# Kernel optimization log

Measured on AMD Instinct MI355X. Metric: run time of the kernel, lower is better.

## Reference

```python
import jax, jax.numpy as jnp
import numpy as np

N = 100000      # nodes
E = 1600000     # directed edges
LAT = 128
MAT = 8
OUT = 3


def setup_inputs() -> dict:
    key = jax.random.key(0)
    ks = jax.random.split(key, 5)
    z = jax.random.normal(ks[0], (N, LAT), dtype=jnp.float32)
    material_params = jax.random.normal(ks[1], (N, MAT), dtype=jnp.float32)
    edge_index = jax.random.randint(ks[2], (2, E), 0, N, dtype=jnp.int64)
    W1 = jax.random.normal(ks[3], (LAT + MAT, LAT), dtype=jnp.float32) * 0.05
    b1 = jnp.zeros((LAT,), dtype=jnp.float32)
    W2 = jax.random.normal(ks[4], (LAT, OUT), dtype=jnp.float32) * 0.05
    b2 = jnp.zeros((OUT,), dtype=jnp.float32)
    return {"z": z, "edge_index": edge_index, "material_params": material_params,
            "W1": W1, "b1": b1, "W2": W2, "b2": b2}


def _gcn_norm(edge_index, num_nodes):
    # PyG GCNConv default: add self-loops, symmetric normalization
    src, dst = edge_index[0], edge_index[1]
    loop = jnp.arange(num_nodes, dtype=src.dtype)
    row = jnp.concatenate([src, loop])  # message source
    col = jnp.concatenate([dst, loop])  # message target
    deg = jax.ops.segment_sum(jnp.ones_like(col, dtype=jnp.float32), col,
                              num_segments=num_nodes)
    dinv = jnp.where(deg > 0, jax.lax.rsqrt(deg), 0.0)
    norm = dinv[row] * dinv[col]        # [E + N]
    return row, col, norm


def _gcn_conv(x, W, b, row, col, norm, num_nodes):
    h = x @ W                                   # linear first (PyG order)
    msg = h[row] * norm[:, None]                # gather + scale
    agg = jax.ops.segment_sum(msg, col, num_segments=num_nodes)
    return agg + b


def reference(z, edge_index, material_params, W1, b1, W2, b2):
    row, col, norm = _gcn_norm(edge_index, N)
    x = jnp.concatenate([z, material_params], axis=1)     # [N, LAT+MAT]
    x = jax.nn.relu(_gcn_conv(x, W1, b1, row, col, norm, N))
    x = _gcn_conv(x, W2, b2, row, col, norm, N)           # [N, OUT]
    return x
```

## Files before the change

### kernel.cpp

```cpp
#include <hip/hip_runtime.h>

#define N_NODES 100000
#define N_EDGES 1600000
#define LAT 128
#define MAT 8
#define OUTC 3

#define NBKT 391
#define CAP  4608
#define CHUNK 4096
#define NPART 8

typedef __attribute__((ext_vector_type(8))) short bf16x8;
typedef __attribute__((ext_vector_type(4))) float f32x4;

__device__ __forceinline__ unsigned short bf16r(float f) {
    unsigned int u = __float_as_uint(f);
    u = (u + 0x7fffu + ((u >> 16) & 1u)) >> 16;
    return (unsigned short)u;
}
__device__ __forceinline__ float bf16f(unsigned short h) {
    return __uint_as_float((unsigned int)h << 16);
}

__global__ __launch_bounds__(256) void k_binA(const int* __restrict__ src,
                                              const int* __restrict__ dst,
                                              int* __restrict__ gcount,
                                              unsigned int* __restrict__ binned) {
    __shared__ int hist[NBKT];
    __shared__ int adj[NBKT];
    __shared__ int cur[NBKT];
    __shared__ int wsum[4];
    __shared__ unsigned int lbuf[CHUNK];
    __shared__ unsigned short lbkt[CHUNK];

    int t = threadIdx.x;
    int base = blockIdx.x * CHUNK;
    int nEdge = min(CHUNK, N_EDGES - base);

    for (int i = t; i < NBKT; i += 256) hist[i] = 0;
    __syncthreads();

    unsigned int pk[16];
    unsigned short bk[16];
#pragma unroll
    for (int j = 0; j < 16; ++j) {
        int li = j * 256 + t;
        if (li < nEdge) {
            int e = base + li;
            int d = dst[e];
            int s = src[e];
            pk[j] = ((unsigned int)s << 8) | (unsigned int)(d & 255);
            bk[j] = (unsigned short)(d >> 8);
            atomicAdd(&hist[bk[j]], 1);
        } else {
            bk[j] = 0xffffu;
        }
    }
    __syncthreads();

    int lane = t & 63, w = t >> 6;
    int i0 = 2 * t, i1 = 2 * t + 1;
    int h0 = (i0 < NBKT) ? hist[i0] : 0;
    int h1 = (i1 < NBKT) ? hist[i1] : 0;
    int ps = h0 + h1;
    int x = ps;
#pragma unroll
    for (int off = 1; off < 64; off <<= 1) {
        int y = __shfl_up(x, off, 64);
        if (lane >= off) x += y;
    }
    if (lane == 63) wsum[w] = x;
    __syncthreads();
    int woff = 0;
#pragma unroll
    for (int i = 0; i < 4; ++i)
        if (i < w) woff += wsum[i];
    int excl = woff + x - ps;
    if (i0 < NBKT) {
        int g0 = i0 * CAP + atomicAdd(&gcount[i0], h0);
        adj[i0] = g0 - excl;
        cur[i0] = excl;
    }
    if (i1 < NBKT) {
        int g1r = i1 * CAP + atomicAdd(&gcount[i1], h1);
        adj[i1] = g1r - (excl + h0);
        cur[i1] = excl + h0;
    }
    __syncthreads();

#pragma unroll
    for (int j = 0; j < 16; ++j) {
        if (bk[j] != 0xffffu) {
            int pos = atomicAdd(&cur[bk[j]], 1);
            lbuf[pos] = pk[j];
            lbkt[pos] = bk[j];
        }
    }
    __syncthreads();

    for (int i = t; i < nEdge; i += 256) {
        int b = lbkt[i];
        binned[adj[b] + i] = lbuf[i];
    }
}

__global__ __launch_bounds__(256) void k_bscan(const int* __restrict__ gcount,
                                               int* __restrict__ bucketBase,
                                               int* __restrict__ rowptr) {
    __shared__ int wsum[4];
    int t = threadIdx.x;
    int lane = t & 63, w = t >> 6;
    int i0 = 2 * t, i1 = 2 * t + 1;
    int h0 = (i0 < NBKT) ? gcount[i0] : 0;
    int h1 = (i1 < NBKT) ? gcount[i1] : 0;
    int ps = h0 + h1;
    int x = ps;
#pragma unroll
    for (int off = 1; off < 64; off <<= 1) {
        int y = __shfl_up(x, off, 64);
        if (lane >= off) x += y;
    }
    if (lane == 63) wsum[w] = x;
    __syncthreads();
    int woff = 0;
#pragma unroll
    for (int i = 0; i < 4; ++i)
        if (i < w) woff += wsum[i];
    int excl = woff + x - ps;
    bucketBase[i0] = excl;
    bucketBase[i1] = excl + h0;
    if (t == 0) rowptr[N_NODES] = N_EDGES;
}

__global__ __launch_bounds__(256) void k_binB(const unsigned int* __restrict__ binned,
                                              const int* __restrict__ gcount,
                                              const int* __restrict__ bucketBase,
                                              int* __restrict__ colsrc,
                                              int* __restrict__ rowptr,
                                              float* __restrict__ dinv) {
    __shared__ unsigned int lbuf[CAP];
    __shared__ int lsrc[CAP];
    __shared__ int hist[256];
    __shared__ int cur[256];
    __shared__ int wsum[4];

    int b = blockIdx.x, t = threadIdx.x;
    int cnt = min(gcount[b], CAP);
    int gb = bucketBase[b];
    const unsigned int* bp = binned + (size_t)b * CAP;

    for (int i = t; i < cnt; i += 256) lbuf[i] = bp[i];
    hist[t] = 0;
    __syncthreads();
    for (int i = t; i < cnt; i += 256) atomicAdd(&hist[lbuf[i] & 255], 1);
    __syncthreads();

    int lane = t & 63, w = t >> 6;
    int h = hist[t];
    int x = h;
#pragma unroll
    for (int off = 1; off < 64; off <<= 1) {
        int y = __shfl_up(x, off, 64);
        if (lane >= off) x += y;
    }
    if (lane == 63) wsum[w] = x;
    __syncthreads();
    int woff = 0;
#pragma unroll
    for (int i = 0; i < 4; ++i)
        if (i < w) woff += wsum[i];
    int excl = woff + x - h;
    cur[t] = excl;

    int node = b * 256 + t;
    if (node < N_NODES) {
        rowptr[node] = gb + excl;
        dinv[node] = rsqrtf((float)h + 1.0f);
    }
    __syncthreads();

    for (int i = t; i < cnt; i += 256) {
        unsigned int p = lbuf[i];
        int pos = atomicAdd(&cur[p & 255], 1);
        lsrc[pos] = (int)(p >> 8);
    }
    __syncthreads();

    for (int i = t; i < cnt; i += 256) colsrc[gb + i] = lsrc[i];
}

__global__ void k_wsplit(const float* __restrict__ W1,
                         unsigned short* __restrict__ w1h,
                         unsigned short* __restrict__ w1l) {
    int i = blockIdx.x * 256 + threadIdx.x;
    if (i >= 160 * 128) return;
    int k = i >> 7;
    float w = (k < LAT + MAT) ? W1[i] : 0.f;
    unsigned short h = bf16r(w);
    w1h[i] = h;
    w1l[i] = bf16r(w - bf16f(h));
}

__global__ __launch_bounds__(256) void k_gemm1m(const float* __restrict__ z,
                                                const float* __restrict__ mat,
                                                const unsigned short* __restrict__ w1h,
                                                const unsigned short* __restrict__ w1l,
                                                const float* __restrict__ dinv,
                                                unsigned short* __restrict__ g1p) {
    int wv = threadIdx.x >> 6;
    int l = threadIdx.x & 63;
    int lm = l & 15, q = l >> 4;

    bf16x8 bh[2][5], bl[2][5];
#pragma unroll
    for (int ct = 0; ct < 2; ++ct) {
        int col = (wv * 2 + ct) * 16 + lm;
#pragma unroll
        for (int ks = 0; ks < 5; ++ks) {
#pragma unroll
            for (int j = 0; j < 8; ++j) {
                int k = ks * 32 + q * 8 + j;
                bh[ct][ks][j] = (short)w1h[k * 128 + col];
                bl[ct][ks][j] = (short)w1l[k * 128 + col];
            }
        }
    }

    for (int tile = blockIdx.x; tile < N_NODES / 16; tile += gridDim.x) {
        int n0 = tile * 16;
        int row = n0 + lm;
        f32x4 acc0 = {0.f, 0.f, 0.f, 0.f};
        f32x4 acc1 = {0.f, 0.f, 0.f, 0.f};
#pragma unroll
        for (int ks = 0; ks < 5; ++ks) {
            float a[8];
            if (ks < 4) {
                float4 a0 = *(const float4*)&z[(size_t)row * LAT + ks * 32 + q * 8];
                float4 a1 = *(const float4*)&z[(size_t)row * LAT + ks * 32 + q * 8 + 4];
                a[0] = a0.x; a[1] = a0.y; a[2] = a0.z; a[3] = a0.w;
                a[4] = a1.x; a[5] = a1.y; a[6] = a1.z; a[7] = a1.w;
            } else if (q == 0) {
                float4 m0 = *(const float4*)&mat[(size_t)row * MAT];
                float4 m1 = *(const float4*)&mat[(size_t)row * MAT + 4];
                a[0] = m0.x; a[1] = m0.y; a[2] = m0.z; a[3] = m0.w;
                a[4] = m1.x; a[5] = m1.y; a[6] = m1.z; a[7] = m1.w;
            } else {
#pragma unroll
                for (int j = 0; j < 8; ++j) a[j] = 0.f;
            }
            bf16x8 ah, al;
#pragma unroll
            for (int j = 0; j < 8; ++j) {
                unsigned short h = bf16r(a[j]);
                ah[j] = (short)h;
                al[j] = (short)bf16r(a[j] - bf16f(h));
            }
            acc0 = __builtin_amdgcn_mfma_f32_16x16x32_bf16(ah, bh[0][ks], acc0, 0, 0, 0);
            acc1 = __builtin_amdgcn_mfma_f32_16x16x32_bf16(ah, bh[1][ks], acc1, 0, 0, 0);
            acc0 = __builtin_amdgcn_mfma_f32_16x16x32_bf16(al, bh[0][ks], acc0, 0, 0, 0);
            acc1 = __builtin_amdgcn_mfma_f32_16x16x32_bf16(al, bh[1][ks], acc1, 0, 0, 0);
            acc0 = __builtin_amdgcn_mfma_f32_16x16x32_bf16(ah, bl[0][ks], acc0, 0, 0, 0);
            acc1 = __builtin_amdgcn_mfma_f32_16x16x32_bf16(ah, bl[1][ks], acc1, 0, 0, 0);
        }
#pragma unroll
        for (int r = 0; r < 4; ++r) {
            int m = q * 4 + r;
            float d = dinv[n0 + m];
            g1p[(size_t)(wv * 2 + 0) * (N_NODES * 16) + (size_t)(n0 + m) * 16 + lm] = bf16r(acc0[r] * d);
            g1p[(size_t)(wv * 2 + 1) * (N_NODES * 16) + (size_t)(n0 + m) * 16 + lm] = bf16r(acc1[r] * d);
        }
    }
}

__global__ __launch_bounds__(256) void k_gather1p(const unsigned int* __restrict__ g1p,
                                                  const int* __restrict__ colsrc,
                                                  const int* __restrict__ rowptr,
                                                  const float* __restrict__ dinv,
                                                  const float* __restrict__ b1,
                                                  const float* __restrict__ W2,
                                                  float4* __restrict__ pp) {
    int p = blockIdx.x & 7;
    int nb = blockIdx.x >> 3;
    int wv = threadIdx.x >> 6;
    int l = threadIdx.x & 63;
    int j = l >> 3;
    int c = l & 7;
    int n = nb * 32 + wv * 8 + j;

    const unsigned int* slab = g1p + (size_t)p * (N_NODES * 8);

    unsigned int su = slab[(unsigned)n * 8u + c];
    float ax = __uint_as_float(su << 16);
    float ay = __uint_as_float(su & 0xffff0000u);

    int eBeg = rowptr[n];
    int deg = rowptr[n + 1] - eBeg;

    int degMax = deg;
    degMax = max(degMax, __shfl_xor(degMax, 8, 64));
    degMax = max(degMax, __shfl_xor(degMax, 16, 64));
    degMax = max(degMax, __shfl_xor(degMax, 32, 64));

    for (int k0 = 0; k0 < degMax; k0 += 8) {
        int s0s[8];
#pragma unroll
        for (int q = 0; q < 8; ++q) {
            int k = k0 + q;
            int e = (k < deg) ? (eBeg + k) : 0;
            s0s[q] = colsrc[e];
        }
#pragma unroll
        for (int q = 0; q < 8; ++q) {
            bool act = (k0 + q) < deg;
            int s = act ? s0s[q] : n;
            unsigned int u = slab[(unsigned)s * 8u + c];
            u = act ? u : 0u;
            ax += __uint_as_float(u << 16);
            ay += __uint_as_float(u & 0xffff0000u);
        }
    }

    float d = dinv[n];
    int r = p * 16 + 2 * c;
    float2 bb = *(const float2*)&b1[r];
    float x0 = fmaxf(ax * d + bb.x, 0.f);
    float x1 = fmaxf(ay * d + bb.y, 0.f);
    float p0 = x0 * W2[r * 3 + 0] + x1 * W2[r * 3 + 3];
    float p1 = x0 * W2[r * 3 + 1] + x1 * W2[r * 3 + 4];
    float p2 = x0 * W2[r * 3 + 2] + x1 * W2[r * 3 + 5];

    p0 += __shfl_xor(p0, 1, 64); p1 += __shfl_xor(p1, 1, 64); p2 += __shfl_xor(p2, 1, 64);
    p0 += __shfl_xor(p0, 2, 64); p1 += __shfl_xor(p1, 2, 64); p2 += __shfl_xor(p2, 2, 64);
    p0 += __shfl_xor(p0, 4, 64); p1 += __shfl_xor(p1, 4, 64); p2 += __shfl_xor(p2, 4, 64);

    if (c == 0) pp[(size_t)p * N_NODES + n] = make_float4(p0, p1, p2, 0.f);
}

__global__ void k_g2build(const float4* __restrict__ pp, const float* __restrict__ dinv,
                          float4* __restrict__ g2) {
    int n = blockIdx.x * blockDim.x + threadIdx.x;
    if (n >= N_NODES) return;
    float s0 = 0.f, s1 = 0.f, s2 = 0.f;
#pragma unroll
    for (int p = 0; p < NPART; ++p) {
        float4 v = pp[(size_t)p * N_NODES + n];
        s0 += v.x; s1 += v.y; s2 += v.z;
    }
    float d = dinv[n];
    g2[n] = make_float4(s0 * d, s1 * d, s2 * d, 0.f);
}

__global__ void k_gather2(const float* __restrict__ g2, const int* __restrict__ colsrc,
                          const int* __restrict__ rowptr, const float* __restrict__ dinv,
                          const float* __restrict__ b2, float* __restrict__ out) {
    int n = blockIdx.x * blockDim.x + threadIdx.x;
    if (n >= N_NODES) return;
    const float4* gv = (const float4*)g2;
    float4 a = gv[n];
    float s0 = a.x, s1 = a.y, s2 = a.z;
    int eEnd = rowptr[n + 1];
    for (int e = rowptr[n]; e < eEnd; ++e) {
        float4 v = gv[colsrc[e]];
        s0 += v.x; s1 += v.y; s2 += v.z;
    }
    float d = dinv[n];
    out[(size_t)n * 3 + 0] = s0 * d + b2[0];
    out[(size_t)n * 3 + 1] = s1 * d + b2[1];
    out[(size_t)n * 3 + 2] = s2 * d + b2[2];
}


extern "C" void kernel_launch(void* const* d_in, const int* in_sizes, int n_in,
                              void* d_out, int out_size, void* d_ws, size_t ws_size,
                              hipStream_t stream) {
    const float* z   = (const float*)d_in[0];
    const int*   ei  = (const int*)d_in[1];
    const float* mat = (const float*)d_in[2];
    const float* W1  = (const float*)d_in[3];
    const float* b1  = (const float*)d_in[4];
    const float* W2  = (const float*)d_in[5];
    const float* b2  = (const float*)d_in[6];
    float* out = (float*)d_out;

    const int* srcA = ei;
    const int* dstA = ei + N_EDGES;

    char* ws = (char*)d_ws;
    auto alloc = [&](size_t bytes) {
        char* p = ws;
        ws += (bytes + 255) & ~(size_t)255;
        return p;
    };
    int*   gcount     = (int*)alloc(512 * 4);
    int*   bucketBase = (int*)alloc(512 * 4);
    int*   rowptr     = (int*)alloc((size_t)(N_NODES + 1) * 4);
    float* dinv       = (float*)alloc((size_t)N_NODES * 4);
    int*   colsrc     = (int*)alloc((size_t)N_EDGES * 4);
    unsigned short* g1p = (unsigned short*)alloc((size_t)NPART * N_NODES * 16 * 2);
    float4* pp        = (float4*)alloc((size_t)NPART * N_NODES * 16);
    float* g2         = (float*)alloc((size_t)N_NODES * 4 * 4);
    unsigned short* w1h = (unsigned short*)alloc(160 * 128 * 2);
    unsigned short* w1l = (unsigned short*)alloc(160 * 128 * 2);
    unsigned int* binned = (unsigned int*)g1p;

    hipMemsetAsync(gcount, 0, 512 * 4, stream);
    int nBlocksA = (N_EDGES + CHUNK - 1) / CHUNK;
    k_binA<<<nBlocksA, 256, 0, stream>>>(srcA, dstA, gcount, binned);
    k_bscan<<<1, 256, 0, stream>>>(gcount, bucketBase, rowptr);
    k_binB<<<NBKT, 256, 0, stream>>>(binned, gcount, bucketBase, colsrc, rowptr, dinv);
    k_wsplit<<<(160 * 128 + 255) / 256, 256, 0, stream>>>(W1, w1h, w1l);
    k_gemm1m<<<1250, 256, 0, stream>>>(z, mat, w1h, w1l, dinv, g1p);
    k_gather1p<<<NPART * (N_NODES / 32), 256, 0, stream>>>((const unsigned int*)g1p, colsrc,
                                                           rowptr, dinv, b1, W2, pp);
    k_g2build<<<(N_NODES + 255) / 256, 256, 0, stream>>>(pp, dinv, (float4*)g2);
    k_gather2<<<(N_NODES + 255) / 256, 256, 0, stream>>>(g2, colsrc, rowptr, dinv, b2, out);
}
```

Baseline: 188.1 us.

## Sort nodes by degree for layer-1 gather and widen per-lane loads to uint2

Adds a degree histogram, scan and scatter that build a permutation grouping nodes by in-degree (capped at 63). The layer-1 gather then walks nodes in this order, so each wave holds nodes of similar degree and spends fewer idle iterations padding up to the wave's maximum degree. Each lane now loads 8 bytes (4 bf16 channels) instead of 4, so a wave covers 16 nodes rather than 8. Partial results are indexed by permuted position and un-permuted in g2build. The cost is three extra small kernels, atomic contention on the 64-bin histogram, and a scattered node order that loses locality for the self and row-pointer reads.

After: 752.1 us. 4x slower.

```diff
diff --git a/kernel.cpp b/kernel.cpp
--- a/kernel.cpp
+++ b/kernel.cpp
@@ -10,6 +10,7 @@
 #define CAP  4608
 #define CHUNK 4096
 #define NPART 8
+#define NPOS  100032
 
 typedef __attribute__((ext_vector_type(8))) short bf16x8;
 typedef __attribute__((ext_vector_type(4))) float f32x4;
@@ -22,6 +23,8 @@
 __device__ __forceinline__ float bf16f(unsigned short h) {
     return __uint_as_float((unsigned int)h << 16);
 }
+__device__ __forceinline__ float bf16lo(unsigned int u) { return __uint_as_float(u << 16); }
+__device__ __forceinline__ float bf16hi(unsigned int u) { return __uint_as_float(u & 0xffff0000u); }
 
 __global__ __launch_bounds__(256) void k_binA(const int* __restrict__ src,
                                               const int* __restrict__ dst,
@@ -188,6 +191,38 @@
     __syncthreads();
 
     for (int i = t; i < cnt; i += 256) colsrc[gb + i] = lsrc[i];
+}
+
+__global__ void k_dhist(const int* __restrict__ rowptr, int* __restrict__ dh) {
+    int n = blockIdx.x * 256 + threadIdx.x;
+    if (n < N_NODES) {
+        int deg = rowptr[n + 1] - rowptr[n];
+        atomicAdd(&dh[min(deg, 63)], 1);
+    }
+}
+
+__global__ void k_dscan(const int* __restrict__ dh, int* __restrict__ dcur,
+                        int* __restrict__ perm) {
+    int t = threadIdx.x;
+    int v = dh[t];
+    int x = v;
+#pragma unroll
+    for (int off = 1; off < 64; off <<= 1) {
+        int y = __shfl_up(x, off, 64);
+        if (t >= off) x += y;
+    }
+    dcur[t] = x - v;
+    if (t < NPOS - N_NODES) perm[N_NODES + t] = 0;
+}
+
+__global__ void k_dscatter(const int* __restrict__ rowptr, int* __restrict__ dcur,
+                           int* __restrict__ perm) {
+    int n = blockIdx.x * 256 + threadIdx.x;
+    if (n < N_NODES) {
+        int deg = rowptr[n + 1] - rowptr[n];
+        int pos = atomicAdd(&dcur[min(deg, 63)], 1);
+        perm[pos] = n;
+    }
 }
 
 __global__ void k_wsplit(const float* __restrict__ W1,
@@ -273,9 +308,10 @@
     }
 }
 
-__global__ __launch_bounds__(256) void k_gather1p(const unsigned int* __restrict__ g1p,
+__global__ __launch_bounds__(256) void k_gather1p(const uint2* __restrict__ slabs,
                                                   const int* __restrict__ colsrc,
                                                   const int* __restrict__ rowptr,
+                                                  const int* __restrict__ perm,
                                                   const float* __restrict__ dinv,
                                                   const float* __restrict__ b1,
                                                   const float* __restrict__ W2,
@@ -284,67 +320,73 @@
     int nb = blockIdx.x >> 3;
     int wv = threadIdx.x >> 6;
     int l = threadIdx.x & 63;
-    int j = l >> 3;
-    int c = l & 7;
-    int n = nb * 32 + wv * 8 + j;
-
-    const unsigned int* slab = g1p + (size_t)p * (N_NODES * 8);
-
-    unsigned int su = slab[(unsigned)n * 8u + c];
-    float ax = __uint_as_float(su << 16);
-    float ay = __uint_as_float(su & 0xffff0000u);
+    int j = l >> 2;
+    int c = l & 3;
+    int i = nb * 64 + wv * 16 + j;
+    int n = perm[i];
+
+    const uint2* slab = slabs + (size_t)p * (N_NODES * 4);
+
+    uint2 su = slab[(unsigned)n * 4u + c];
+    float a0 = bf16lo(su.x), a1 = bf16hi(su.x);
+    float a2 = bf16lo(su.y), a3 = bf16hi(su.y);
 
     int eBeg = rowptr[n];
     int deg = rowptr[n + 1] - eBeg;
 
     int degMax = deg;
+    degMax = max(degMax, __shfl_xor(degMax, 4, 64));
     degMax = max(degMax, __shfl_xor(degMax, 8, 64));
     degMax = max(degMax, __shfl_xor(degMax, 16, 64));
     degMax = max(degMax, __shfl_xor(degMax, 32, 64));
 
     for (int k0 = 0; k0 < degMax; k0 += 8) {
-        int s0s[8];
+        int ss[8];
 #pragma unroll
         for (int q = 0; q < 8; ++q) {
             int k = k0 + q;
-            int e = (k < deg) ? (eBeg + k) : 0;
-            s0s[q] = colsrc[e];
+            int e = eBeg + ((k < deg) ? k : 0);
+            int s = colsrc[e];
+            ss[q] = (k < deg) ? s : n;
         }
 #pragma unroll
         for (int q = 0; q < 8; ++q) {
+            uint2 u = slab[(unsigned)ss[q] * 4u + c];
             bool act = (k0 + q) < deg;
-            int s = act ? s0s[q] : n;
-            unsigned int u = slab[(unsigned)s * 8u + c];
-            u = act ? u : 0u;
-            ax += __uint_as_float(u << 16);
-            ay += __uint_as_float(u & 0xffff0000u);
+            u.x = act ? u.x : 0u;
+            u.y = act ? u.y : 0u;
+            a0 += bf16lo(u.x); a1 += bf16hi(u.x);
+            a2 += bf16lo(u.y); a3 += bf16hi(u.y);
         }
     }
 
     float d = dinv[n];
-    int r = p * 16 + 2 * c;
-    float2 bb = *(const float2*)&b1[r];
-    float x0 = fmaxf(ax * d + bb.x, 0.f);
-    float x1 = fmaxf(ay * d + bb.y, 0.f);
-    float p0 = x0 * W2[r * 3 + 0] + x1 * W2[r * 3 + 3];
-    float p1 = x0 * W2[r * 3 + 1] + x1 * W2[r * 3 + 4];
-    float p2 = x0 * W2[r * 3 + 2] + x1 * W2[r * 3 + 5];
+    int r = p * 16 + 4 * c;
+    float4 bb = *(const float4*)&b1[r];
+    float x0 = fmaxf(a0 * d + bb.x, 0.f);
+    float x1 = fmaxf(a1 * d + bb.y, 0.f);
+    float x2 = fmaxf(a2 * d + bb.z, 0.f);
+    float x3 = fmaxf(a3 * d + bb.w, 0.f);
+    const float* w2r = W2 + r * 3;
+    float p0 = x0 * w2r[0] + x1 * w2r[3] + x2 * w2r[6] + x3 * w2r[9];
+    float p1 = x0 * w2r[1] + x1 * w2r[4] + x2 * w2r[7] + x3 * w2r[10];
+    float p2 = x0 * w2r[2] + x1 * w2r[5] + x2 * w2r[8] + x3 * w2r[11];
 
     p0 += __shfl_xor(p0, 1, 64); p1 += __shfl_xor(p1, 1, 64); p2 += __shfl_xor(p2, 1, 64);
     p0 += __shfl_xor(p0, 2, 64); p1 += __shfl_xor(p1, 2, 64); p2 += __shfl_xor(p2, 2, 64);
-    p0 += __shfl_xor(p0, 4, 64); p1 += __shfl_xor(p1, 4, 64); p2 += __shfl_xor(p2, 4, 64);
-
-    if (c == 0) pp[(size_t)p * N_NODES + n] = make_float4(p0, p1, p2, 0.f);
-}
-
-__global__ void k_g2build(const float4* __restrict__ pp, const float* __restrict__ dinv,
-                          float4* __restrict__ g2) {
-    int n = blockIdx.x * blockDim.x + threadIdx.x;
-    if (n >= N_NODES) return;
+
+    if (c == 0) pp[(size_t)p * NPOS + i] = make_float4(p0, p1, p2, 0.f);
+}
+
+__global__ void k_g2build(const float4* __restrict__ pp, const int* __restrict__ perm,
+                          const float* __restrict__ dinv, float4* __restrict__ g2) {
+    int i = blockIdx.x * blockDim.x + threadIdx.x;
+    if (i >= N_NODES) return;
+    int n = perm[i];
     float s0 = 0.f, s1 = 0.f, s2 = 0.f;
 #pragma unroll
     for (int p = 0; p < NPART; ++p) {
-        float4 v = pp[(size_t)p * N_NODES + n];
+        float4 v = pp[(size_t)p * NPOS + i];
         s0 += v.x; s1 += v.y; s2 += v.z;
     }
     float d = dinv[n];
@@ -396,23 +438,30 @@
     int*   bucketBase = (int*)alloc(512 * 4);
     int*   rowptr     = (int*)alloc((size_t)(N_NODES + 1) * 4);
     float* dinv       = (float*)alloc((size_t)N_NODES * 4);
-    int*   colsrc     = (int*)alloc((size_t)N_EDGES * 4);
+    int*   colsrc     = (int*)alloc((size_t)N_EDGES * 4 + 256);
     unsigned short* g1p = (unsigned short*)alloc((size_t)NPART * N_NODES * 16 * 2);
-    float4* pp        = (float4*)alloc((size_t)NPART * N_NODES * 16);
+    float4* pp        = (float4*)alloc((size_t)NPART * NPOS * 16);
     float* g2         = (float*)alloc((size_t)N_NODES * 4 * 4);
     unsigned short* w1h = (unsigned short*)alloc(160 * 128 * 2);
     unsigned short* w1l = (unsigned short*)alloc(160 * 128 * 2);
+    int*   perm       = (int*)alloc((size_t)NPOS * 4);
+    int*   dh         = (int*)alloc(64 * 4);
+    int*   dcur       = (int*)alloc(64 * 4);
     unsigned int* binned = (unsigned int*)g1p;
 
     hipMemsetAsync(gcount, 0, 512 * 4, stream);
+    hipMemsetAsync(dh, 0, 64 * 4, stream);
     int nBlocksA = (N_EDGES + CHUNK - 1) / CHUNK;
     k_binA<<<nBlocksA, 256, 0, stream>>>(srcA, dstA, gcount, binned);
     k_bscan<<<1, 256, 0, stream>>>(gcount, bucketBase, rowptr);
     k_binB<<<NBKT, 256, 0, stream>>>(binned, gcount, bucketBase, colsrc, rowptr, dinv);
+    k_dhist<<<(N_NODES + 255) / 256, 256, 0, stream>>>(rowptr, dh);
+    k_dscan<<<1, 64, 0, stream>>>(dh, dcur, perm);
+    k_dscatter<<<(N_NODES + 255) / 256, 256, 0, stream>>>(rowptr, dcur, perm);
     k_wsplit<<<(160 * 128 + 255) / 256, 256, 0, stream>>>(W1, w1h, w1l);
     k_gemm1m<<<1250, 256, 0, stream>>>(z, mat, w1h, w1l, dinv, g1p);
-    k_gather1p<<<NPART * (N_NODES / 32), 256, 0, stream>>>((const unsigned int*)g1p, colsrc,
-                                                           rowptr, dinv, b1, W2, pp);
-    k_g2build<<<(N_NODES + 255) / 256, 256, 0, stream>>>(pp, dinv, (float4*)g2);
+    k_gather1p<<<NPART * (NPOS / 64), 256, 0, stream>>>((const uint2*)g1p, colsrc, rowptr,
+                                                        perm, dinv, b1, W2, pp);
+    k_g2build<<<(N_NODES + 255) / 256, 256, 0, stream>>>(pp, perm, dinv, (float4*)g2);
     k_gather2<<<(N_NODES + 255) / 256, 256, 0, stream>>>(g2, colsrc, rowptr, dinv, b2, out);
 }
```
